# Performance work log

Measured on AMD Instinct MI355X. Metric: run time of the kernel, lower is better.

## Reference

```python
import jax, jax.numpy as jnp
import numpy as np

D_MODEL = 2048
NUM_HEADS = 16
HEAD_DIM = D_MODEL // NUM_HEADS  # 128; scale uses head_dim even though attention is over full d_model
B, S = 2, 2048


def setup_inputs() -> dict:
    key = jax.random.key(0)
    ks = jax.random.split(key, 5)
    x = jax.random.normal(ks[0], (B, S, D_MODEL), dtype=jnp.float32)
    # causal additive mask, as typically passed to this module (2D, sliced mask[-s:, :kv])
    neg = jnp.float32(-1e9)
    mask = jnp.where(jnp.triu(jnp.ones((S, S), dtype=bool), k=1), neg, jnp.float32(0.0))
    std = 1.0 / np.sqrt(D_MODEL)
    Wq = jax.random.normal(ks[1], (D_MODEL, D_MODEL), dtype=jnp.float32) * std
    Wk = jax.random.normal(ks[2], (D_MODEL, D_MODEL), dtype=jnp.float32) * std
    Wv = jax.random.normal(ks[3], (D_MODEL, D_MODEL), dtype=jnp.float32) * std
    Wo = jax.random.normal(ks[4], (D_MODEL, D_MODEL), dtype=jnp.float32) * std
    return {"x": x, "mask": mask, "Wq": Wq, "Wk": Wk, "Wv": Wv, "Wo": Wo}


def reference(x, mask, Wq, Wk, Wv, Wo):
    # nn.Linear(bias=False): y = x @ W^T
    q = jnp.einsum('bsd,ed->bse', x, Wq)  # [B,S,D]
    k = jnp.einsum('bsd,ed->bse', x, Wk)
    v = jnp.einsum('bsd,ed->bse', x, Wv)
    scale = jnp.float32(HEAD_DIM ** -0.5)
    # NOTE: faithful to source — contraction over full d_model, no head split
    scores = jnp.einsum('bsd,btd->bst', q, k) * scale  # [B,S,S]
    scores = scores + mask  # mask[-s:, :kv] == mask here (s == kv)
    weights = jax.nn.softmax(scores, axis=-1)
    out = jnp.einsum('bst,btd->bsd', weights, v)
    return jnp.einsum('bsd,ed->bse', out, Wo)
```

## Files before the change

kernel.cpp:

```cpp
#include <hip/hip_runtime.h>

#define DM  2048
#define SQ  2048
#define NB  2
#define BSZ (NB * SQ)

typedef _Float16 f16x8 __attribute__((ext_vector_type(8)));
typedef __attribute__((ext_vector_type(4))) float f32x4;

#define ASG(p) (const __attribute__((address_space(1))) void*)(p)
#define ASL(p) (__attribute__((address_space(3))) void*)(p)

__device__ __forceinline__ unsigned short f2h(float f) {
  union { _Float16 h; unsigned short u; } x;
  x.h = (_Float16)f;
  return x.u;
}
__device__ __forceinline__ float h2f(unsigned short u) {
  union { unsigned short u; _Float16 h; } x;
  x.u = u;
  return (float)x.h;
}

__global__ __launch_bounds__(256) void cast_all(const float4* __restrict__ x,
                                                const float4* __restrict__ wq,
                                                const float4* __restrict__ wk,
                                                const float4* __restrict__ wv,
                                                const float4* __restrict__ wo,
                                                ushort4* __restrict__ out,
                                                int n4x, int n4w) {
  int i = blockIdx.x * 256 + threadIdx.x;
  float4 v;
  if (i < n4x) {
    v = x[i];
  } else {
    int j = i - n4x;
    int seg = j >> 20;
    int off = j & (n4w - 1);
    const float4* src = (seg == 0) ? wq : (seg == 1) ? wk : (seg == 2) ? wv : wo;
    v = src[off];
  }
  ushort4 h;
  h.x = f2h(v.x); h.y = f2h(v.y); h.z = f2h(v.z); h.w = f2h(v.w);
  out[i] = h;
}

#define SB() __builtin_amdgcn_sched_barrier(0)
#define BARX() do { SB(); __builtin_amdgcn_s_barrier(); SB(); } while (0)

#define STAGE8(BUFL, HALF, T) do { \
    const unsigned short* G_ = ((HALF) < 2) ? Ab : Bb; \
    const int ldG_ = ((HALF) < 2) ? ldA : ldB; \
    const int r0_ = (((HALF) < 2) ? bm0 : bn0) + ((HALF) & 1) * 128; \
    const long k0_ = (long)((T) << 6); \
    char* db_ = ldsb + (BUFL) * 65536 + (HALF) * 16384 + tid * 16; \
    const unsigned short* s0_ = G_ + (long)(r0_ + srow) * ldG_ + k0_ + scsw; \
    const unsigned short* s1_ = G_ + (long)(r0_ + 64 + srow) * ldG_ + k0_ + scsw; \
    __builtin_amdgcn_global_load_lds(ASG(s0_), ASL(db_), 16, 0, 0); \
    __builtin_amdgcn_global_load_lds(ASG(s1_), ASL(db_ + 8192), 16, 0, 0); \
  } while (0)

#define LDA8(BUFL, MQ, Af) do { \
    const char* ba_ = ldsb + (BUFL) * 65536 + wm * 16384 + (MQ) * 8192 + arow; \
    _Pragma("unroll") for (int mm_ = 0; mm_ < 4; mm_++) { \
      Af[mm_][0] = *(const f16x8*)(ba_ + mm_ * 2048 + sl0); \
      Af[mm_][1] = *(const f16x8*)(ba_ + mm_ * 2048 + sl1); } \
  } while (0)

#define LDB8(BUFL, NQ, Bf) do { \
    const char* bb_ = ldsb + (BUFL) * 65536 + 32768 + (wn * 2 + (NQ)) * 4096 + arow; \
    _Pragma("unroll") for (int nn_ = 0; nn_ < 2; nn_++) { \
      Bf[nn_][0] = *(const f16x8*)(bb_ + nn_ * 2048 + sl0); \
      Bf[nn_][1] = *(const f16x8*)(bb_ + nn_ * 2048 + sl1); } \
  } while (0)

#define PH8(Af, Bf, MQ, NQ) do { \
    __builtin_amdgcn_s_setprio(1); \
    _Pragma("unroll") for (int mm_ = 0; mm_ < 4; mm_++) \
    _Pragma("unroll") for (int nn_ = 0; nn_ < 2; nn_++) \
    _Pragma("unroll") for (int ks_ = 0; ks_ < 2; ks_++) \
      acc[(MQ) * 4 + mm_][(NQ) * 2 + nn_] = __builtin_amdgcn_mfma_f32_16x16x32_f16( \
          Af[mm_][ks_], Bf[nn_][ks_], acc[(MQ) * 4 + mm_][(NQ) * 2 + nn_], 0, 0, 0); \
    __builtin_amdgcn_s_setprio(0); \
  } while (0)

#define GROUP8(BUFL, T) do { \
    LDA8(BUFL, 0, a0); LDB8(BUFL, 0, b0); \
    LDA8(BUFL, 1, a1); \
    if ((T) + 1 < NT) STAGE8(BUFL ^ 1, 3, (T) + 1); \
    PH8(a0, b0, 0, 0); \
    BARX(); \
    LDB8(BUFL, 1, b1); \
    PH8(a1, b0, 1, 0); \
    BARX(); \
    if ((T) + 2 < NT) STAGE8(BUFL, 0, (T) + 2); \
    PH8(a1, b1, 1, 1); \
    BARX(); \
    if ((T) + 2 < NT) { STAGE8(BUFL, 1, (T) + 2); STAGE8(BUFL, 2, (T) + 2); } \
    PH8(a0, b1, 0, 1); \
    SB(); \
    if ((T) + 1 < NT) { \
      if ((T) + 1 == NT - 1) { asm volatile("s_waitcnt vmcnt(0)" ::: "memory"); } \
      else                   { asm volatile("s_waitcnt vmcnt(6)" ::: "memory"); } \
    } \
    __builtin_amdgcn_s_barrier(); \
    SB(); \
  } while (0)

template <int OM>
__global__ __launch_bounds__(512, 2) void gemm8p(
    const unsigned short* __restrict__ A, const unsigned short* __restrict__ B,
    float* __restrict__ Cf, unsigned short* __restrict__ Ch,
    int K, int ldA, int ldB, int ldC) {
  __shared__ __align__(16) char ldsarr[131072];
  char* ldsb = ldsarr;

  const int bm0 = blockIdx.x * 256;
  const int bn0 = blockIdx.y * 256;
  const unsigned short* Ab = A;
  const unsigned short* Bb = B;

  const int tid = threadIdx.x, lane = tid & 63, wid = tid >> 6;
  const int wm = wid >> 2, wn = wid & 3;
  const int fr = lane & 15, fq = lane >> 4;
  const int NT = K >> 6;

  const int sl0 = ((fq ^ (fr & 7)) << 4);
  const int sl1 = (((4 + fq) ^ (fr & 7)) << 4);
  const int arow = fr << 7;

  const int srow = tid >> 3;
  const int scsw = ((tid & 7) ^ (srow & 7)) << 3;

  f32x4 acc[8][4];
#pragma unroll
  for (int m = 0; m < 8; m++)
#pragma unroll
    for (int n = 0; n < 4; n++)
#pragma unroll
      for (int r = 0; r < 4; r++) acc[m][n][r] = 0.f;

  f16x8 a0[4][2], a1[4][2], b0[2][2], b1[2][2];

  STAGE8(0, 0, 0); STAGE8(0, 1, 0); STAGE8(0, 2, 0); STAGE8(0, 3, 0);
  STAGE8(1, 0, 1); STAGE8(1, 1, 1); STAGE8(1, 2, 1);
  asm volatile("s_waitcnt vmcnt(6)" ::: "memory");
  __builtin_amdgcn_s_barrier();
  SB();

  for (int t = 0; t < NT; t += 2) {
    GROUP8(0, t);
    GROUP8(1, t + 1);
  }

#pragma unroll
  for (int mq = 0; mq < 2; mq++)
#pragma unroll
    for (int mm = 0; mm < 4; mm++)
#pragma unroll
      for (int nq = 0; nq < 2; nq++)
#pragma unroll
        for (int nn = 0; nn < 2; nn++) {
          const int col = bn0 + wn * 64 + nq * 32 + nn * 16 + fr;
#pragma unroll
          for (int r = 0; r < 4; r++) {
            const long row = (long)bm0 + wm * 128 + mq * 64 + mm * 16 + fq * 4 + r;
            const long ci = row * ldC + col;
            if constexpr (OM == 0) Cf[ci] = acc[mq * 4 + mm][nq * 2 + nn][r];
            else                   Ch[ci] = f2h(acc[mq * 4 + mm][nq * 2 + nn][r]);
          }
        }
}

#define STAGER(BUFL, REG, U, T) do { \
    const unsigned short* G_ = (REG) ? Bb : Ab; \
    const int ldG_ = (REG) ? ldB : ldA; \
    const int r0_ = ((REG) ? bn0 : bm0) + (U) * 64; \
    const long k0_ = (long)((T) << 6); \
    char* db_ = ldsb + (BUFL) * 49152 + (REG) * 16384 + (U) * 8192 + tid * 16; \
    const unsigned short* s_ = G_ + (long)(r0_ + srow) * ldG_ + k0_ + scsw; \
    __builtin_amdgcn_global_load_lds(ASG(s_), ASL(db_), 16, 0, 0); \
  } while (0)

#define LDAR(BUFL, MH, Af) do { \
    const char* ba_ = ldsb + (BUFL) * 49152 + (wm * 64 + (MH) * 32) * 128 + arow; \
    _Pragma("unroll") for (int mm_ = 0; mm_ < 2; mm_++) { \
      Af[mm_][0] = *(const f16x8*)(ba_ + mm_ * 2048 + sl0); \
      Af[mm_][1] = *(const f16x8*)(ba_ + mm_ * 2048 + sl1); } \
  } while (0)

#define LDBR(BUFL, NH, Bf) do { \
    const char* bb_ = ldsb + (BUFL) * 49152 + 16384 + (wn * 64 + (NH) * 32) * 128 + arow; \
    _Pragma("unroll") for (int nn_ = 0; nn_ < 2; nn_++) { \
      Bf[nn_][0] = *(const f16x8*)(bb_ + nn_ * 2048 + sl0); \
      Bf[nn_][1] = *(const f16x8*)(bb_ + nn_ * 2048 + sl1); } \
  } while (0)

#define PHR(Af, Bf, MH, NH) do { \
    __builtin_amdgcn_s_setprio(1); \
    _Pragma("unroll") for (int mm_ = 0; mm_ < 2; mm_++) \
    _Pragma("unroll") for (int nn_ = 0; nn_ < 2; nn_++) \
    _Pragma("unroll") for (int ks_ = 0; ks_ < 2; ks_++) \
      acc[(MH) * 2 + mm_][(NH) * 2 + nn_] = __builtin_amdgcn_mfma_f32_16x16x32_f16( \
          Af[mm_][ks_], Bf[nn_][ks_], acc[(MH) * 2 + mm_][(NH) * 2 + nn_], 0, 0, 0); \
    __builtin_amdgcn_s_setprio(0); \
  } while (0)

#define GROUPR(BUFL, T) do { \
    LDAR(BUFL, 0, a0); LDBR(BUFL, 0, b0); \
    LDAR(BUFL, 1, a1); \
    if ((T) + 1 < NT) STAGER(BUFL ^ 1, 1, 3, (T) + 1); \
    PHR(a0, b0, 0, 0); \
    BARX(); \
    LDBR(BUFL, 1, b1); \
    PHR(a1, b0, 1, 0); \
    BARX(); \
    if ((T) + 2 < NT) { STAGER(BUFL, 0, 0, (T) + 2); STAGER(BUFL, 0, 1, (T) + 2); } \
    PHR(a1, b1, 1, 1); \
    BARX(); \
    if ((T) + 2 < NT) { STAGER(BUFL, 1, 0, (T) + 2); STAGER(BUFL, 1, 1, (T) + 2); STAGER(BUFL, 1, 2, (T) + 2); } \
    PHR(a0, b1, 0, 1); \
    SB(); \
    if ((T) + 1 < NT) { \
      if ((T) + 1 == NT - 1) { asm volatile("s_waitcnt vmcnt(0)" ::: "memory"); } \
      else                   { asm volatile("s_waitcnt vmcnt(5)" ::: "memory"); } \
    } \
    __builtin_amdgcn_s_barrier(); \
    SB(); \
  } while (0)

template <int OM, int CAUSAL>
__global__ __launch_bounds__(512, 2) void gemm8pR(
    const unsigned short* __restrict__ A, const unsigned short* __restrict__ B,
    float* __restrict__ Cf, unsigned short* __restrict__ Ch,
    int K, long sAb, long sBb, long sCb,
    int ldA, int ldB, int ldC, float alpha) {
  __shared__ __align__(16) char ldsarr[98304];
  char* ldsb = ldsarr;

  const int bm0 = blockIdx.x * 128;
  const int bn0 = blockIdx.y * 256;
  if (CAUSAL == 1 && bn0 > bm0 + 127) return;

  const int z = blockIdx.z;
  const unsigned short* Ab = A + (long)z * sAb;
  const unsigned short* Bb = B + (long)z * sBb;
  const long cb = (long)z * sCb;

  const int tid = threadIdx.x, lane = tid & 63, wid = tid >> 6;
  const int wm = wid >> 2, wn = wid & 3;
  const int fr = lane & 15, fq = lane >> 4;
  int NT = K >> 6;
  if (CAUSAL == 2) NT = (bm0 + 128) >> 6;

  const int sl0 = ((fq ^ (fr & 7)) << 4);
  const int sl1 = (((4 + fq) ^ (fr & 7)) << 4);
  const int arow = fr << 7;

  const int srow = tid >> 3;
  const int scsw = ((tid & 7) ^ (srow & 7)) << 3;

  f32x4 acc[4][4];
#pragma unroll
  for (int m = 0; m < 4; m++)
#pragma unroll
    for (int n = 0; n < 4; n++)
#pragma unroll
      for (int r = 0; r < 4; r++) acc[m][n][r] = 0.f;

  f16x8 a0[2][2], a1[2][2], b0[2][2], b1[2][2];

  STAGER(0, 0, 0, 0); STAGER(0, 0, 1, 0);
  STAGER(0, 1, 0, 0); STAGER(0, 1, 1, 0); STAGER(0, 1, 2, 0); STAGER(0, 1, 3, 0);
  STAGER(1, 0, 0, 1); STAGER(1, 0, 1, 1);
  STAGER(1, 1, 0, 1); STAGER(1, 1, 1, 1); STAGER(1, 1, 2, 1);
  asm volatile("s_waitcnt vmcnt(5)" ::: "memory");
  __builtin_amdgcn_s_barrier();
  SB();

  for (int t = 0; t < NT; t += 2) {
    GROUPR(0, t);
    GROUPR(1, t + 1);
  }

#pragma unroll
  for (int mh = 0; mh < 2; mh++)
#pragma unroll
    for (int mm = 0; mm < 2; mm++)
#pragma unroll
      for (int nh = 0; nh < 2; nh++)
#pragma unroll
        for (int nn = 0; nn < 2; nn++) {
          const int col = bn0 + wn * 64 + nh * 32 + nn * 16 + fr;
#pragma unroll
          for (int r = 0; r < 4; r++) {
            const long row = (long)bm0 + wm * 64 + mh * 32 + mm * 16 + fq * 4 + r;
            const long ci = cb + row * ldC + col;
            const float vv = acc[mh * 2 + mm][nh * 2 + nn][r] * alpha;
            if constexpr (OM == 0) Cf[ci] = vv;
            else                   Ch[ci] = f2h(vv);
          }
        }
}

__global__ __launch_bounds__(256) void softmax_causal(const unsigned short* __restrict__ sc,
                                                      unsigned short* __restrict__ pr) {
  const int row = blockIdx.x;
  const int s = row & (SQ - 1);
  const long base = (long)row * SQ;
  const int n = s + 1;
  const int tid = threadIdx.x;
  const int lane = tid & 63;
  const int wv = tid >> 6;
  const int e0 = tid * 8;
  __shared__ float red[4];

  union { uint4 u4; unsigned short us[8]; } in, ou;
  in.u4 = *(const uint4*)&sc[base + e0];

  float v[8];
  float mx = -3.0e38f;
#pragma unroll
  for (int j = 0; j < 8; j++) {
    v[j] = (e0 + j < n) ? h2f(in.us[j]) : -3.0e38f;
    mx = fmaxf(mx, v[j]);
  }
#pragma unroll
  for (int o = 32; o >= 1; o >>= 1) mx = fmaxf(mx, __shfl_xor(mx, o));
  if (lane == 0) red[wv] = mx;
  __syncthreads();
  mx = fmaxf(fmaxf(red[0], red[1]), fmaxf(red[2], red[3]));
  __syncthreads();

  float sum = 0.f;
#pragma unroll
  for (int j = 0; j < 8; j++) {
    v[j] = (e0 + j < n) ? __expf(v[j] - mx) : 0.f;
    sum += v[j];
  }
#pragma unroll
  for (int o = 32; o >= 1; o >>= 1) sum += __shfl_xor(sum, o);
  if (lane == 0) red[wv] = sum;
  __syncthreads();
  const float inv = 1.f / (red[0] + red[1] + red[2] + red[3]);
#pragma unroll
  for (int j = 0; j < 8; j++) ou.us[j] = (e0 + j < n) ? f2h(v[j] * inv) : (unsigned short)0;
  *(uint4*)&pr[base + e0] = ou.u4;
}

extern "C" void kernel_launch(void* const* d_in, const int* in_sizes, int n_in,
                              void* d_out, int out_size, void* d_ws, size_t ws_size,
                              hipStream_t stream) {
  (void)in_sizes; (void)n_in; (void)out_size; (void)ws_size;
  const float* x  = (const float*)d_in[0];
  const float* Wq = (const float*)d_in[2];
  const float* Wk = (const float*)d_in[3];
  const float* Wv = (const float*)d_in[4];
  const float* Wo = (const float*)d_in[5];
  float* out = (float*)d_out;

  const long ELx = (long)BSZ * DM;
  const long ELw = (long)DM * DM;

  char* ws = (char*)d_ws;
  size_t off = 0;
  auto take = [&](size_t bytes) { void* p = ws + off; off += bytes; return p; };

  unsigned short* x16   = (unsigned short*)take(ELx * 2);
  unsigned short* wqk16 = (unsigned short*)take(2 * ELw * 2);
  unsigned short* wv16  = (unsigned short*)take(ELw * 2);
  unsigned short* wo16  = (unsigned short*)take(ELw * 2);
  unsigned short* qk16  = (unsigned short*)take((long)BSZ * 2 * DM * 2);
  unsigned short* vTT   = (unsigned short*)take(ELx * 2);
  unsigned short* probs = (unsigned short*)take((long)NB * SQ * SQ * 2);
  unsigned short* scores = x16;
  unsigned short* ctx = qk16;
  unsigned short* q16 = qk16;
  unsigned short* k16 = qk16 + DM;

  const int n4x = (int)(ELx / 4), n4w = (int)(ELw / 4);
  cast_all<<<dim3((n4x + 4 * n4w) / 256), 256, 0, stream>>>(
      (const float4*)x, (const float4*)Wq, (const float4*)Wk,
      (const float4*)Wv, (const float4*)Wo, (ushort4*)x16, n4x, n4w);

  const float scale = 0.08838834764831845f;

  gemm8p<1><<<dim3(BSZ / 256, 2 * DM / 256), 512, 0, stream>>>(
      x16, wqk16, nullptr, qk16, DM, DM, DM, 2 * DM);
  gemm8pR<1, 0><<<dim3(DM / 128, BSZ / 256, 1), 512, 0, stream>>>(
      wv16, x16, nullptr, vTT, DM, 0L, 0L, 0L, DM, DM, BSZ, 1.0f);
  gemm8pR<1, 1><<<dim3(SQ / 128, SQ / 256, NB), 512, 0, stream>>>(
      q16, k16, nullptr, scores, DM, (long)SQ * 2 * DM, (long)SQ * 2 * DM,
      (long)SQ * SQ, 2 * DM, 2 * DM, SQ, scale);

  softmax_causal<<<dim3(NB * SQ), 256, 0, stream>>>(scores, probs);

  gemm8pR<1, 2><<<dim3(SQ / 128, DM / 256, NB), 512, 0, stream>>>(
      probs, vTT, nullptr, ctx, SQ, (long)SQ * SQ, 2048L, (long)SQ * DM,
      SQ, BSZ, DM, 1.0f);
  gemm8pR<0, 0><<<dim3(BSZ / 128, DM / 256, 1), 512, 0, stream>>>(
      ctx, wo16, out, nullptr, DM, 0L, 0L, 0L, DM, DM, DM, 1.0f);
}
```

Baseline: 240.3 us.

## Replace 256x256 and 128x256 GEMM kernels with unified 128x128 tile kernel

All five GEMMs now go through one 128x128-tile kernel with 256 threads (4 waves of 64x64) and 64KB LDS double buffering, replacing the 256x256/512-thread QK projection kernel and the 128x256 kernel. Smaller tiles give more blocks and finer causal skipping in the scores GEMM, which may help load balance and occupancy. In exchange, each tile reuses less data, so global and LDS traffic per FLOP rises, and the staging and wait counts were re-tuned for the new layout.

```diff
diff --git a/kernel.cpp b/kernel.cpp
--- a/kernel.cpp
+++ b/kernel.cpp
@@ -48,56 +48,55 @@
 #define SB() __builtin_amdgcn_sched_barrier(0)
 #define BARX() do { SB(); __builtin_amdgcn_s_barrier(); SB(); } while (0)
 
-#define STAGE8(BUFL, HALF, T) do { \
-    const unsigned short* G_ = ((HALF) < 2) ? Ab : Bb; \
-    const int ldG_ = ((HALF) < 2) ? ldA : ldB; \
-    const int r0_ = (((HALF) < 2) ? bm0 : bn0) + ((HALF) & 1) * 128; \
+#define STAGEK(BUFL, REG, U, T) do { \
+    const unsigned short* G_ = (REG) ? Bb : Ab; \
+    const int ldG_ = (REG) ? ldB : ldA; \
+    const int r0_ = ((REG) ? bn0 : bm0) + (U) * 32; \
     const long k0_ = (long)((T) << 6); \
-    char* db_ = ldsb + (BUFL) * 65536 + (HALF) * 16384 + tid * 16; \
-    const unsigned short* s0_ = G_ + (long)(r0_ + srow) * ldG_ + k0_ + scsw; \
-    const unsigned short* s1_ = G_ + (long)(r0_ + 64 + srow) * ldG_ + k0_ + scsw; \
-    __builtin_amdgcn_global_load_lds(ASG(s0_), ASL(db_), 16, 0, 0); \
-    __builtin_amdgcn_global_load_lds(ASG(s1_), ASL(db_ + 8192), 16, 0, 0); \
-  } while (0)
-
-#define LDA8(BUFL, MQ, Af) do { \
-    const char* ba_ = ldsb + (BUFL) * 65536 + wm * 16384 + (MQ) * 8192 + arow; \
-    _Pragma("unroll") for (int mm_ = 0; mm_ < 4; mm_++) { \
+    char* db_ = ldsb + (BUFL) * 32768 + (REG) * 16384 + (U) * 4096 + tid * 16; \
+    const unsigned short* s_ = G_ + (long)(r0_ + srow) * ldG_ + k0_ + scsw; \
+    __builtin_amdgcn_global_load_lds(ASG(s_), ASL(db_), 16, 0, 0); \
+  } while (0)
+
+#define LDAK(BUFL, MH, Af) do { \
+    const char* ba_ = ldsb + (BUFL) * 32768 + (wm * 64 + (MH) * 32) * 128 + arow; \
+    _Pragma("unroll") for (int mm_ = 0; mm_ < 2; mm_++) { \
       Af[mm_][0] = *(const f16x8*)(ba_ + mm_ * 2048 + sl0); \
       Af[mm_][1] = *(const f16x8*)(ba_ + mm_ * 2048 + sl1); } \
   } while (0)
 
-#define LDB8(BUFL, NQ, Bf) do { \
-    const char* bb_ = ldsb + (BUFL) * 65536 + 32768 + (wn * 2 + (NQ)) * 4096 + arow; \
+#define LDBK(BUFL, NH, Bf) do { \
+    const char* bb_ = ldsb + (BUFL) * 32768 + 16384 + (wn * 64 + (NH) * 32) * 128 + arow; \
     _Pragma("unroll") for (int nn_ = 0; nn_ < 2; nn_++) { \
       Bf[nn_][0] = *(const f16x8*)(bb_ + nn_ * 2048 + sl0); \
       Bf[nn_][1] = *(const f16x8*)(bb_ + nn_ * 2048 + sl1); } \
   } while (0)
 
-#define PH8(Af, Bf, MQ, NQ) do { \
+#define PHK(Af, Bf, MH, NH) do { \
     __builtin_amdgcn_s_setprio(1); \
-    _Pragma("unroll") for (int mm_ = 0; mm_ < 4; mm_++) \
+    _Pragma("unroll") for (int mm_ = 0; mm_ < 2; mm_++) \
     _Pragma("unroll") for (int nn_ = 0; nn_ < 2; nn_++) \
     _Pragma("unroll") for (int ks_ = 0; ks_ < 2; ks_++) \
-      acc[(MQ) * 4 + mm_][(NQ) * 2 + nn_] = __builtin_amdgcn_mfma_f32_16x16x32_f16( \
-          Af[mm_][ks_], Bf[nn_][ks_], acc[(MQ) * 4 + mm_][(NQ) * 2 + nn_], 0, 0, 0); \
+      acc[(MH) * 2 + mm_][(NH) * 2 + nn_] = __builtin_amdgcn_mfma_f32_16x16x32_f16( \
+          Af[mm_][ks_], Bf[nn_][ks_], acc[(MH) * 2 + mm_][(NH) * 2 + nn_], 0, 0, 0); \
     __builtin_amdgcn_s_setprio(0); \
   } while (0)
 
-#define GROUP8(BUFL, T) do { \
-    LDA8(BUFL, 0, a0); LDB8(BUFL, 0, b0); \
-    LDA8(BUFL, 1, a1); \
-    if ((T) + 1 < NT) STAGE8(BUFL ^ 1, 3, (T) + 1); \
-    PH8(a0, b0, 0, 0); \
+#define GROUPK(BUFL, T) do { \
+    LDAK(BUFL, 0, a0); LDBK(BUFL, 0, b0); \
+    LDAK(BUFL, 1, a1); \
+    if ((T) + 1 < NT) { STAGEK((BUFL) ^ 1, 1, 2, (T) + 1); STAGEK((BUFL) ^ 1, 1, 3, (T) + 1); } \
+    PHK(a0, b0, 0, 0); \
     BARX(); \
-    LDB8(BUFL, 1, b1); \
-    PH8(a1, b0, 1, 0); \
+    LDBK(BUFL, 1, b1); \
+    PHK(a1, b0, 1, 0); \
     BARX(); \
-    if ((T) + 2 < NT) STAGE8(BUFL, 0, (T) + 2); \
-    PH8(a1, b1, 1, 1); \
+    if ((T) + 2 < NT) { STAGEK(BUFL, 0, 0, (T) + 2); STAGEK(BUFL, 0, 1, (T) + 2); \
+                        STAGEK(BUFL, 0, 2, (T) + 2); STAGEK(BUFL, 0, 3, (T) + 2); } \
+    PHK(a1, b1, 1, 1); \
     BARX(); \
-    if ((T) + 2 < NT) { STAGE8(BUFL, 1, (T) + 2); STAGE8(BUFL, 2, (T) + 2); } \
-    PH8(a0, b1, 0, 1); \
+    if ((T) + 2 < NT) { STAGEK(BUFL, 1, 0, (T) + 2); STAGEK(BUFL, 1, 1, (T) + 2); } \
+    PHK(a0, b1, 0, 1); \
     SB(); \
     if ((T) + 1 < NT) { \
       if ((T) + 1 == NT - 1) { asm volatile("s_waitcnt vmcnt(0)" ::: "memory"); } \
@@ -107,140 +106,18 @@
     SB(); \
   } while (0)
 
-template <int OM>
-__global__ __launch_bounds__(512, 2) void gemm8p(
-    const unsigned short* __restrict__ A, const unsigned short* __restrict__ B,
-    float* __restrict__ Cf, unsigned short* __restrict__ Ch,
-    int K, int ldA, int ldB, int ldC) {
-  __shared__ __align__(16) char ldsarr[131072];
-  char* ldsb = ldsarr;
-
-  const int bm0 = blockIdx.x * 256;
-  const int bn0 = blockIdx.y * 256;
-  const unsigned short* Ab = A;
-  const unsigned short* Bb = B;
-
-  const int tid = threadIdx.x, lane = tid & 63, wid = tid >> 6;
-  const int wm = wid >> 2, wn = wid & 3;
-  const int fr = lane & 15, fq = lane >> 4;
-  const int NT = K >> 6;
-
-  const int sl0 = ((fq ^ (fr & 7)) << 4);
-  const int sl1 = (((4 + fq) ^ (fr & 7)) << 4);
-  const int arow = fr << 7;
-
-  const int srow = tid >> 3;
-  const int scsw = ((tid & 7) ^ (srow & 7)) << 3;
-
-  f32x4 acc[8][4];
-#pragma unroll
-  for (int m = 0; m < 8; m++)
-#pragma unroll
-    for (int n = 0; n < 4; n++)
-#pragma unroll
-      for (int r = 0; r < 4; r++) acc[m][n][r] = 0.f;
-
-  f16x8 a0[4][2], a1[4][2], b0[2][2], b1[2][2];
-
-  STAGE8(0, 0, 0); STAGE8(0, 1, 0); STAGE8(0, 2, 0); STAGE8(0, 3, 0);
-  STAGE8(1, 0, 1); STAGE8(1, 1, 1); STAGE8(1, 2, 1);
-  asm volatile("s_waitcnt vmcnt(6)" ::: "memory");
-  __builtin_amdgcn_s_barrier();
-  SB();
-
-  for (int t = 0; t < NT; t += 2) {
-    GROUP8(0, t);
-    GROUP8(1, t + 1);
-  }
-
-#pragma unroll
-  for (int mq = 0; mq < 2; mq++)
-#pragma unroll
-    for (int mm = 0; mm < 4; mm++)
-#pragma unroll
-      for (int nq = 0; nq < 2; nq++)
-#pragma unroll
-        for (int nn = 0; nn < 2; nn++) {
-          const int col = bn0 + wn * 64 + nq * 32 + nn * 16 + fr;
-#pragma unroll
-          for (int r = 0; r < 4; r++) {
-            const long row = (long)bm0 + wm * 128 + mq * 64 + mm * 16 + fq * 4 + r;
-            const long ci = row * ldC + col;
-            if constexpr (OM == 0) Cf[ci] = acc[mq * 4 + mm][nq * 2 + nn][r];
-            else                   Ch[ci] = f2h(acc[mq * 4 + mm][nq * 2 + nn][r]);
-          }
-        }
-}
-
-#define STAGER(BUFL, REG, U, T) do { \
-    const unsigned short* G_ = (REG) ? Bb : Ab; \
-    const int ldG_ = (REG) ? ldB : ldA; \
-    const int r0_ = ((REG) ? bn0 : bm0) + (U) * 64; \
-    const long k0_ = (long)((T) << 6); \
-    char* db_ = ldsb + (BUFL) * 49152 + (REG) * 16384 + (U) * 8192 + tid * 16; \
-    const unsigned short* s_ = G_ + (long)(r0_ + srow) * ldG_ + k0_ + scsw; \
-    __builtin_amdgcn_global_load_lds(ASG(s_), ASL(db_), 16, 0, 0); \
-  } while (0)
-
-#define LDAR(BUFL, MH, Af) do { \
-    const char* ba_ = ldsb + (BUFL) * 49152 + (wm * 64 + (MH) * 32) * 128 + arow; \
-    _Pragma("unroll") for (int mm_ = 0; mm_ < 2; mm_++) { \
-      Af[mm_][0] = *(const f16x8*)(ba_ + mm_ * 2048 + sl0); \
-      Af[mm_][1] = *(const f16x8*)(ba_ + mm_ * 2048 + sl1); } \
-  } while (0)
-
-#define LDBR(BUFL, NH, Bf) do { \
-    const char* bb_ = ldsb + (BUFL) * 49152 + 16384 + (wn * 64 + (NH) * 32) * 128 + arow; \
-    _Pragma("unroll") for (int nn_ = 0; nn_ < 2; nn_++) { \
-      Bf[nn_][0] = *(const f16x8*)(bb_ + nn_ * 2048 + sl0); \
-      Bf[nn_][1] = *(const f16x8*)(bb_ + nn_ * 2048 + sl1); } \
-  } while (0)
-
-#define PHR(Af, Bf, MH, NH) do { \
-    __builtin_amdgcn_s_setprio(1); \
-    _Pragma("unroll") for (int mm_ = 0; mm_ < 2; mm_++) \
-    _Pragma("unroll") for (int nn_ = 0; nn_ < 2; nn_++) \
-    _Pragma("unroll") for (int ks_ = 0; ks_ < 2; ks_++) \
-      acc[(MH) * 2 + mm_][(NH) * 2 + nn_] = __builtin_amdgcn_mfma_f32_16x16x32_f16( \
-          Af[mm_][ks_], Bf[nn_][ks_], acc[(MH) * 2 + mm_][(NH) * 2 + nn_], 0, 0, 0); \
-    __builtin_amdgcn_s_setprio(0); \
-  } while (0)
-
-#define GROUPR(BUFL, T) do { \
-    LDAR(BUFL, 0, a0); LDBR(BUFL, 0, b0); \
-    LDAR(BUFL, 1, a1); \
-    if ((T) + 1 < NT) STAGER(BUFL ^ 1, 1, 3, (T) + 1); \
-    PHR(a0, b0, 0, 0); \
-    BARX(); \
-    LDBR(BUFL, 1, b1); \
-    PHR(a1, b0, 1, 0); \
-    BARX(); \
-    if ((T) + 2 < NT) { STAGER(BUFL, 0, 0, (T) + 2); STAGER(BUFL, 0, 1, (T) + 2); } \
-    PHR(a1, b1, 1, 1); \
-    BARX(); \
-    if ((T) + 2 < NT) { STAGER(BUFL, 1, 0, (T) + 2); STAGER(BUFL, 1, 1, (T) + 2); STAGER(BUFL, 1, 2, (T) + 2); } \
-    PHR(a0, b1, 0, 1); \
-    SB(); \
-    if ((T) + 1 < NT) { \
-      if ((T) + 1 == NT - 1) { asm volatile("s_waitcnt vmcnt(0)" ::: "memory"); } \
-      else                   { asm volatile("s_waitcnt vmcnt(5)" ::: "memory"); } \
-    } \
-    __builtin_amdgcn_s_barrier(); \
-    SB(); \
-  } while (0)
-
 template <int OM, int CAUSAL>
-__global__ __launch_bounds__(512, 2) void gemm8pR(
+__global__ __launch_bounds__(256, 2) void gemm128(
     const unsigned short* __restrict__ A, const unsigned short* __restrict__ B,
     float* __restrict__ Cf, unsigned short* __restrict__ Ch,
     int K, long sAb, long sBb, long sCb,
     int ldA, int ldB, int ldC, float alpha) {
-  __shared__ __align__(16) char ldsarr[98304];
+  __shared__ __align__(16) char ldsarr[65536];
   char* ldsb = ldsarr;
 
   const int bm0 = blockIdx.x * 128;
-  const int bn0 = blockIdx.y * 256;
-  if (CAUSAL == 1 && bn0 > bm0 + 127) return;
+  const int bn0 = blockIdx.y * 128;
+  if (CAUSAL == 1 && bn0 > bm0) return;
 
   const int z = blockIdx.z;
   const unsigned short* Ab = A + (long)z * sAb;
@@ -248,7 +125,7 @@
   const long cb = (long)z * sCb;
 
   const int tid = threadIdx.x, lane = tid & 63, wid = tid >> 6;
-  const int wm = wid >> 2, wn = wid & 3;
+  const int wm = wid >> 1, wn = wid & 1;
   const int fr = lane & 15, fq = lane >> 4;
   int NT = K >> 6;
   if (CAUSAL == 2) NT = (bm0 + 128) >> 6;
@@ -270,17 +147,17 @@
 
   f16x8 a0[2][2], a1[2][2], b0[2][2], b1[2][2];
 
-  STAGER(0, 0, 0, 0); STAGER(0, 0, 1, 0);
-  STAGER(0, 1, 0, 0); STAGER(0, 1, 1, 0); STAGER(0, 1, 2, 0); STAGER(0, 1, 3, 0);
-  STAGER(1, 0, 0, 1); STAGER(1, 0, 1, 1);
-  STAGER(1, 1, 0, 1); STAGER(1, 1, 1, 1); STAGER(1, 1, 2, 1);
-  asm volatile("s_waitcnt vmcnt(5)" ::: "memory");
+  STAGEK(0, 0, 0, 0); STAGEK(0, 0, 1, 0); STAGEK(0, 0, 2, 0); STAGEK(0, 0, 3, 0);
+  STAGEK(0, 1, 0, 0); STAGEK(0, 1, 1, 0); STAGEK(0, 1, 2, 0); STAGEK(0, 1, 3, 0);
+  STAGEK(1, 0, 0, 1); STAGEK(1, 0, 1, 1); STAGEK(1, 0, 2, 1); STAGEK(1, 0, 3, 1);
+  STAGEK(1, 1, 0, 1); STAGEK(1, 1, 1, 1);
+  asm volatile("s_waitcnt vmcnt(6)" ::: "memory");
   __builtin_amdgcn_s_barrier();
   SB();
 
   for (int t = 0; t < NT; t += 2) {
-    GROUPR(0, t);
-    GROUPR(1, t + 1);
+    GROUPK(0, t);
+    GROUPK(1, t + 1);
   }
 
 #pragma unroll
@@ -385,19 +262,19 @@
 
   const float scale = 0.08838834764831845f;
 
-  gemm8p<1><<<dim3(BSZ / 256, 2 * DM / 256), 512, 0, stream>>>(
-      x16, wqk16, nullptr, qk16, DM, DM, DM, 2 * DM);
-  gemm8pR<1, 0><<<dim3(DM / 128, BSZ / 256, 1), 512, 0, stream>>>(
+  gemm128<1, 0><<<dim3(BSZ / 128, 2 * DM / 128, 1), 256, 0, stream>>>(
+      x16, wqk16, nullptr, qk16, DM, 0L, 0L, 0L, DM, DM, 2 * DM, 1.0f);
+  gemm128<1, 0><<<dim3(DM / 128, BSZ / 128, 1), 256, 0, stream>>>(
       wv16, x16, nullptr, vTT, DM, 0L, 0L, 0L, DM, DM, BSZ, 1.0f);
-  gemm8pR<1, 1><<<dim3(SQ / 128, SQ / 256, NB), 512, 0, stream>>>(
+  gemm128<1, 1><<<dim3(SQ / 128, SQ / 128, NB), 256, 0, stream>>>(
       q16, k16, nullptr, scores, DM, (long)SQ * 2 * DM, (long)SQ * 2 * DM,
       (long)SQ * SQ, 2 * DM, 2 * DM, SQ, scale);
 
   softmax_causal<<<dim3(NB * SQ), 256, 0, stream>>>(scores, probs);
 
-  gemm8pR<1, 2><<<dim3(SQ / 128, DM / 256, NB), 512, 0, stream>>>(
+  gemm128<1, 2><<<dim3(SQ / 128, DM / 128, NB), 256, 0, stream>>>(
       probs, vTT, nullptr, ctx, SQ, (long)SQ * SQ, 2048L, (long)SQ * DM,
       SQ, BSZ, DM, 1.0f);
-  gemm8pR<0, 0><<<dim3(BSZ / 128, DM / 256, 1), 512, 0, stream>>>(
+  gemm128<0, 0><<<dim3(BSZ / 128, DM / 128, 1), 256, 0, stream>>>(
       ctx, wo16, out, nullptr, DM, 0L, 0L, 0L, DM, DM, DM, 1.0f);
 }
```

Result: no change. 240.2 us (-0.0%).
